# Kernel tuning notes

Measured on AMD Instinct MI355X. Metric: run time of the kernel, lower is better.

The kernel has to match this reference:

```python
import jax, jax.numpy as jnp
import numpy as np

N = 4096
IN = 64          # input_size
QD = 16          # query_vector_dim
CI = 2 * IN + 1  # 129, MLP_Param input dim


def _xavier(key, shape):
    fan_in, fan_out = shape[-2], shape[-1]
    bound = float(np.sqrt(6.0 / (fan_in + fan_out)))
    return jax.random.uniform(key, shape, jnp.float32, -bound, bound)


def setup_inputs() -> dict:
    key = jax.random.key(0)
    ks = jax.random.split(key, 10)
    return {
        "x": jax.random.normal(ks[0], (N, IN + 1), jnp.float32),
        "h": jax.random.normal(ks[1], (N, IN), jnp.float32),
        "query_vectors": jax.random.normal(ks[2], (N, QD), jnp.float32),
        "adj": jax.random.uniform(ks[3], (N, N), jnp.float32),
        "nodes_ind": jnp.arange(N, dtype=jnp.int64 if jax.config.jax_enable_x64 else jnp.int32),
        "W_r": _xavier(ks[4], (QD, CI, IN)),
        "b_r": _xavier(ks[5], (QD, IN)),
        "W_u": _xavier(ks[6], (QD, CI, IN)),
        "b_u": _xavier(ks[7], (QD, IN)),
        "W_c": _xavier(ks[8], (QD, CI, IN)),
        "b_c": _xavier(ks[9], (QD, IN)),
    }


def _mlp_param(xv, q, W, b):
    # per-node dynamic weights: [n, CI, IN]
    Wn = jnp.einsum('nd,dio->nio', q, W)
    return jnp.einsum('ni,nio->no', xv, Wn) + q @ b


def reference(x, h, query_vectors, adj, nodes_ind, W_r, b_r, W_u, b_u, W_c, b_c):
    combined = adj @ jnp.concatenate([x, h], axis=-1)          # [N, 129]
    cg = combined[nodes_ind]                                    # [M, 129]
    r = jax.nn.sigmoid(_mlp_param(cg, query_vectors, W_r, b_r))
    u = jax.nn.sigmoid(_mlp_param(cg, query_vectors, W_u, b_u))
    h2 = h.at[nodes_ind].set(r * h[nodes_ind])                  # h[nodes_ind] = r*h[nodes_ind]
    combined_new = jnp.concatenate([x, h2], axis=-1)[nodes_ind]  # no adj mixing second time
    cand = jnp.tanh(_mlp_param(combined_new, query_vectors, W_c, b_c))
    return (1.0 - u) * h2[nodes_ind] + u * cand
```

## Files before the change

kernel.cpp:

```cpp
#include <hip/hip_runtime.h>
#include <math.h>


#define NN   4096
#define XCC  65
#define HCC  64
#define QDIM 16
#define CI   129
#define CST  132
#define AKST 520
#define GSTRIDE 147456

typedef unsigned short u16;
typedef __attribute__((ext_vector_type(4))) unsigned short ushort4_t;
typedef __attribute__((ext_vector_type(8))) unsigned short ushort8_t;
typedef __attribute__((ext_vector_type(8))) short bf16x8;
typedef __attribute__((ext_vector_type(16))) float f32x16;

__device__ __forceinline__ void split2(float a, u16& hi, u16& lo) {
  unsigned u = __float_as_uint(a);
  hi = (u16)(u >> 16);
  float rec = __uint_as_float(u & 0xFFFF0000u);
  float lf = a - rec;
  unsigned v = __float_as_uint(lf);
  v += 0x7FFF + ((v >> 16) & 1);
  lo = (u16)(v >> 16);
}

__device__ __forceinline__ void gload_lds16(const void* gsrc, void* ldst) {
  __builtin_amdgcn_global_load_lds(
      (const __attribute__((address_space(1))) unsigned int*)gsrc,
      (__attribute__((address_space(3))) unsigned int*)ldst, 16, 0, 0);
}

__global__ __launch_bounds__(256) void k0_pack(const float* __restrict__ x,
                                               const float* __restrict__ h,
                                               u16* __restrict__ Bh,
                                               u16* __restrict__ Bl,
                                               const float* __restrict__ Wr,
                                               const float* __restrict__ Wu,
                                               const float* __restrict__ Wc,
                                               u16* __restrict__ Wh,
                                               u16* __restrict__ Wl) {
  __shared__ float sT[64][161];
  const int t = threadIdx.x;
  if (blockIdx.x < 64) {
    const int n0 = blockIdx.x * 64;
    for (int f = t; f < 64 * XCC; f += 256) {
      int n = f / XCC, c = f - n * XCC;
      sT[n][c] = x[(size_t)(n0 + n) * XCC + c];
    }
    for (int f = t; f < 64 * HCC; f += 256) {
      int n = f >> 6, c = f & 63;
      sT[n][XCC + c] = h[(size_t)(n0 + n) * HCC + c];
    }
    for (int f = t; f < 64 * 31; f += 256) {
      int n = f / 31, c = f - n * 31;
      sT[n][CI + c] = 0.f;
    }
    __syncthreads();
    for (int idx = t; idx < 5 * 4 * 64; idx += 256) {
      const int lane = idx & 63;
      const int ksl = (idx >> 6) & 3;
      const int ct = idx >> 8;
      const int nl = ksl * 16 + (lane >> 5) * 8;
      const int feat = ct * 32 + (lane & 31);
      ushort8_t vh, vl;
#pragma unroll
      for (int j = 0; j < 8; ++j) {
        u16 hi, lo; split2(sT[nl + j][feat], hi, lo);
        vh[j] = hi; vl[j] = lo;
      }
      const size_t off = (((size_t)ct * 256 + (blockIdx.x * 4) + ksl) * 64 + lane) * 8;
      *(ushort8_t*)(Bh + off) = vh;
      *(ushort8_t*)(Bl + off) = vl;
    }
  } else {
    int gid = (blockIdx.x - 64) * 256 + t;
    if (gid >= 3 * 16 * 2 * 9 * 64) return;
    int lane = gid & 63;
    int rest = gid >> 6;
    int kst = rest % 9; rest /= 9;
    int ct = rest & 1; rest >>= 1;
    int d = rest & 15; rest >>= 4;
    const float* W = (rest == 0) ? Wr : (rest == 1 ? Wu : Wc);
    const int o = ct * 32 + (lane & 31);
    const int i0 = kst * 16 + (lane >> 5) * 8;
    ushort8_t vh, vl;
#pragma unroll
    for (int j = 0; j < 8; ++j) {
      int i = i0 + j;
      float v = (i < CI) ? W[((size_t)d * CI + i) * 64 + o] : 0.f;
      u16 hi, lo; split2(v, hi, lo);
      vh[j] = hi; vl[j] = lo;
    }
    const size_t off = (size_t)gid * 8;
    *(ushort8_t*)(Wh + off) = vh;
    *(ushort8_t*)(Wl + off) = vl;
  }
}

template <int SPK>
__global__ __launch_bounds__(256, 4) void k1_mfma(const float* __restrict__ adj,
                                                  const u16* __restrict__ Bh,
                                                  const u16* __restrict__ Bl,
                                                  float* __restrict__ P1) {
  constexpr int KLEN = 4096 / SPK;
  constexpr int STEPS = KLEN / 16;
  __shared__ u16 sAh[2][2][64][8];
  __shared__ u16 sAl[2][2][64][8];
  __shared__ u16 sB[3][10][512];
  __shared__ u16 sScratch[512];
  const int t = threadIdx.x;
  const int lane = t & 63;
  const int w = t >> 6;
  const int rgrp = w & 1;
  const int cthalf = w >> 1;
  const int m0 = blockIdx.x * 64;
  const int sp = blockIdx.y;
  const int ct0 = cthalf ? 3 : 0;
  const int R = t >> 2;
  const int ksts = t & 3;
  const int srg = R >> 5, srl = R & 31;
  const int skh = ksts >> 1, sj0 = (ksts & 1) * 4;

  f32x16 a0, a1, a2;
#pragma unroll
  for (int r = 0; r < 16; ++r) { a0[r] = 0.f; a1[r] = 0.f; a2[r] = 0.f; }

  const float* aptr = adj + (size_t)(m0 + R) * NN + sp * KLEN + ksts * 4;
  float4 va, vb, vc;

#define LOADA(it, tgt) tgt = *(const float4*)(aptr + (it) * 16);

#define CONV4(src, abuf)                                                       \
  {                                                                            \
    u16 h0, h1, h2, h3, l0, l1, l2, l3;                                        \
    split2(src.x, h0, l0); split2(src.y, h1, l1);                              \
    split2(src.z, h2, l2); split2(src.w, h3, l3);                              \
    ushort4_t hv = {h0, h1, h2, h3};                                           \
    ushort4_t lv = {l0, l1, l2, l3};                                           \
    *(ushort4_t*)&sAh[abuf][srg][srl + 32 * skh][sj0] = hv;                    \
    *(ushort4_t*)&sAl[abuf][srg][srl + 32 * skh][sj0] = lv;                    \
  }

#define BDMA(it, bbuf)                                                         \
  {                                                                            \
    _Pragma("unroll")                                                          \
    for (int j = 0; j < 3; ++j) {                                              \
      const int c = w + 4 * j;                                                 \
      const int ct = (c < 10) ? (c >> 1) : 0;                                  \
      const int hl = (c < 10) ? (c & 1) : 0;                                   \
      const int ks = sp * STEPS + (it);                                        \
      const u16* src =                                                         \
          (hl ? Bl : Bh) + (((size_t)ct * 256 + ks) * 64 + lane) * 8;          \
      gload_lds16(src, (c < 10) ? &sB[bbuf][c][0] : &sScratch[0]);             \
    }                                                                          \
  }

#define BAR(N)                                                                 \
  asm volatile("s_waitcnt vmcnt(" #N ") lgkmcnt(0)" ::: "memory");             \
  __builtin_amdgcn_sched_barrier(0);                                           \
  __builtin_amdgcn_s_barrier();                                                \
  __builtin_amdgcn_sched_barrier(0);

#define COMPUTE(abuf, bbuf)                                                    \
  {                                                                            \
    bf16x8 ah = *(const bf16x8*)&sAh[abuf][rgrp][lane][0];                     \
    bf16x8 al = *(const bf16x8*)&sAl[abuf][rgrp][lane][0];                     \
    const int cb = ct0 * 2;                                                    \
    bf16x8 b0h = *(const bf16x8*)&sB[bbuf][cb + 0][lane * 8];                  \
    bf16x8 b0l = *(const bf16x8*)&sB[bbuf][cb + 1][lane * 8];                  \
    bf16x8 b1h = *(const bf16x8*)&sB[bbuf][cb + 2][lane * 8];                  \
    bf16x8 b1l = *(const bf16x8*)&sB[bbuf][cb + 3][lane * 8];                  \
    a0 = __builtin_amdgcn_mfma_f32_32x32x16_bf16(ah, b0h, a0, 0, 0, 0);        \
    a1 = __builtin_amdgcn_mfma_f32_32x32x16_bf16(ah, b1h, a1, 0, 0, 0);        \
    a0 = __builtin_amdgcn_mfma_f32_32x32x16_bf16(al, b0h, a0, 0, 0, 0);        \
    a1 = __builtin_amdgcn_mfma_f32_32x32x16_bf16(al, b1h, a1, 0, 0, 0);        \
    a0 = __builtin_amdgcn_mfma_f32_32x32x16_bf16(ah, b0l, a0, 0, 0, 0);        \
    a1 = __builtin_amdgcn_mfma_f32_32x32x16_bf16(ah, b1l, a1, 0, 0, 0);        \
    if (cthalf == 0) {                                                         \
      bf16x8 b2h = *(const bf16x8*)&sB[bbuf][cb + 4][lane * 8];                \
      bf16x8 b2l = *(const bf16x8*)&sB[bbuf][cb + 5][lane * 8];                \
      a2 = __builtin_amdgcn_mfma_f32_32x32x16_bf16(ah, b2h, a2, 0, 0, 0);      \
      a2 = __builtin_amdgcn_mfma_f32_32x32x16_bf16(al, b2h, a2, 0, 0, 0);      \
      a2 = __builtin_amdgcn_mfma_f32_32x32x16_bf16(ah, b2l, a2, 0, 0, 0);      \
    }                                                                          \
  }

  LOADA(0, va);
  BDMA(0, 0);
  LOADA(1, vb);
  BDMA(1, 1);
  LOADA(2, vc);
  CONV4(va, 0);
  BAR(5)
#pragma unroll
  for (int it = 0; it < STEPS; ++it) {
    const int abuf = it & 1;
    const int bbuf = it % 3;
    if (it < STEPS - 2) BDMA(it + 2, (it + 2) % 3);
    if (it <= STEPS - 4) {
      if ((it % 3) == 0) { LOADA(it + 3, va); }
      else if ((it % 3) == 1) { LOADA(it + 3, vb); }
      else { LOADA(it + 3, vc); }
    }
    COMPUTE(abuf, bbuf);
    if (it < STEPS - 1) {
      if (((it + 1) % 3) == 0) { CONV4(va, abuf ^ 1); }
      else if (((it + 1) % 3) == 1) { CONV4(vb, abuf ^ 1); }
      else { CONV4(vc, abuf ^ 1); }
    }
    if (it <= STEPS - 4) { BAR(5) }
    else if (it == STEPS - 3) { BAR(4) }
    else if (it == STEPS - 2) { BAR(0) }
  }
#undef LOADA
#undef CONV4
#undef BDMA
#undef BAR
#undef COMPUTE
  float* outp = P1 + (size_t)sp * NN * CST;
  const int colb = lane & 31;
  const int rbase = m0 + rgrp * 32 + 4 * (lane >> 5);
  {
    const int colg = ct0 * 32 + colb;
#pragma unroll
    for (int r = 0; r < 16; ++r)
      outp[(size_t)(rbase + (r & 3) + 8 * (r >> 2)) * CST + colg] = a0[r];
  }
  {
    const int colg = (ct0 + 1) * 32 + colb;
    if (colg < CST) {
#pragma unroll
      for (int r = 0; r < 16; ++r)
        outp[(size_t)(rbase + (r & 3) + 8 * (r >> 2)) * CST + colg] = a1[r];
    }
  }
  if (cthalf == 0) {
    const int colg = 64 + colb;
#pragma unroll
    for (int r = 0; r < 16; ++r)
      outp[(size_t)(rbase + (r & 3) + 8 * (r >> 2)) * CST + colg] = a2[r];
  }
}

template <int SPK>
__global__ void k1b_reduce(const float* __restrict__ P1, float* __restrict__ XV) {
  int f = blockIdx.x * 256 + threadIdx.x;
  if (f >= NN * 33) return;
  float sx = 0.f, sy = 0.f, sz = 0.f, sw = 0.f;
#pragma unroll
  for (int sp = 0; sp < SPK; ++sp) {
    float4 v = *(const float4*)(P1 + (size_t)sp * NN * CST + (size_t)f * 4);
    sx += v.x; sy += v.y; sz += v.z; sw += v.w;
  }
  float4 s = {sx, sy, sz, sw};
  *(float4*)(XV + (size_t)f * 4) = s;
}

__global__ __launch_bounds__(512) void k2_fused(const float* __restrict__ XV,
                                                const float* __restrict__ q,
                                                const u16* __restrict__ Wh,
                                                const u16* __restrict__ Wl,
                                                const float* __restrict__ br,
                                                const float* __restrict__ bu,
                                                const float* __restrict__ h,
                                                float* __restrict__ U,
                                                float* __restrict__ H2) {
  __shared__ float sXV[32][144];
  __shared__ u16 sAh[9 * AKST], sAl[9 * AKST];
  __shared__ float sQ[32][16];
  __shared__ float sXfer[8][16][64];
  const int t = threadIdx.x;
  const int n0 = blockIdx.x * 32;
  const int g = blockIdx.y >> 1, ct = blockIdx.y & 1;
  for (int f = t; f < 32 * 33; f += 512) {
    int n = f / 33, c4 = f - n * 33;
    *(float4*)&sXV[n][c4 * 4] = *(const float4*)(XV + (size_t)(n0 + n) * CST + c4 * 4);
  }
  for (int f = t; f < 32 * 3; f += 512) {
    float4 z = {0, 0, 0, 0};
    *(float4*)&sXV[f / 3][132 + (f % 3) * 4] = z;
  }
  if (t < 512) sQ[t >> 4][t & 15] = q[(size_t)(n0 + (t >> 4)) * QDIM + (t & 15)];
  __syncthreads();
  for (int s = t; s < 9 * 64; s += 512) {
    int kst = s >> 6, l = s & 63;
    int row = l & 31, k0 = kst * 16 + (l >> 5) * 8;
    ushort8_t vh, vl;
#pragma unroll
    for (int j = 0; j < 8; ++j) {
      u16 hi, lo; split2(sXV[row][k0 + j], hi, lo);
      vh[j] = hi; vl[j] = lo;
    }
    *(ushort8_t*)&sAh[kst * AKST + l * 8] = vh;
    *(ushort8_t*)&sAl[kst * AKST + l * 8] = vl;
  }
  __syncthreads();
  const int lane = t & 63, dh = t >> 6;
  const u16* WhG = Wh + (size_t)g * GSTRIDE;
  const u16* WlG = Wl + (size_t)g * GSTRIDE;
  f32x16 acc;
#pragma unroll
  for (int r = 0; r < 16; ++r) acc[r] = 0.f;
#pragma unroll
  for (int dd = 0; dd < 2; ++dd) {
    const int d = dh * 2 + dd;
    const size_t bb = (((size_t)d * 2 + ct) * 9 * 64 + lane) * 8;
    f32x16 t0, t1, t2;
#pragma unroll
    for (int r = 0; r < 16; ++r) { t0[r] = 0.f; t1[r] = 0.f; t2[r] = 0.f; }
#pragma unroll
    for (int kst = 0; kst < 9; ++kst) {
      bf16x8 ah = *(const bf16x8*)&sAh[kst * AKST + lane * 8];
      bf16x8 al = *(const bf16x8*)&sAl[kst * AKST + lane * 8];
      bf16x8 bh = *(const bf16x8*)(WhG + bb + kst * 512);
      bf16x8 bl = *(const bf16x8*)(WlG + bb + kst * 512);
      t0 = __builtin_amdgcn_mfma_f32_32x32x16_bf16(ah, bh, t0, 0, 0, 0);
      t1 = __builtin_amdgcn_mfma_f32_32x32x16_bf16(al, bh, t1, 0, 0, 0);
      t2 = __builtin_amdgcn_mfma_f32_32x32x16_bf16(ah, bl, t2, 0, 0, 0);
    }
#pragma unroll
    for (int r = 0; r < 16; ++r) {
      int node = (r & 3) + 8 * (r >> 2) + 4 * (lane >> 5);
      acc[r] += sQ[node][d] * (t0[r] + t1[r] + t2[r]);
    }
  }
#pragma unroll
  for (int r = 0; r < 16; ++r) sXfer[dh][r][lane] = acc[r];
  __syncthreads();
  if (dh == 0) {
    const int colb = ct * 32 + (lane & 31);
    const float* bias = (g == 0) ? br : bu;
    float bcol[16];
#pragma unroll
    for (int d = 0; d < 16; ++d) bcol[d] = bias[d * 64 + colb];
#pragma unroll
    for (int r = 0; r < 16; ++r) {
      int node = (r & 3) + 8 * (r >> 2) + 4 * (lane >> 5);
      float pre = 0.f;
#pragma unroll
      for (int wv = 0; wv < 8; ++wv) pre += sXfer[wv][r][lane];
#pragma unroll
      for (int d = 0; d < 16; ++d) pre += sQ[node][d] * bcol[d];
      float sg = 1.f / (1.f + expf(-pre));
      int gidx = (n0 + node) * 64 + colb;
      if (g == 0) H2[gidx] = sg * h[gidx];
      else U[gidx] = sg;
    }
  }
}

__global__ __launch_bounds__(512) void k3_fused(const float* __restrict__ x,
                                                const float* __restrict__ H2,
                                                const float* __restrict__ q,
                                                const u16* __restrict__ Wh,
                                                const u16* __restrict__ Wl,
                                                const float* __restrict__ bc,
                                                const float* __restrict__ U,
                                                float* __restrict__ out) {
  __shared__ float sXV[32][144];
  __shared__ u16 sAh[9 * AKST], sAl[9 * AKST];
  __shared__ float sQ[32][16];
  __shared__ float sXfer[8][16][64];
  const int t = threadIdx.x;
  const int n0 = blockIdx.x * 32;
  const int ct = blockIdx.y;
  for (int f = t; f < 32 * 144; f += 512) {
    int n = f / 144, i = f - n * 144;
    float v = 0.f;
    if (i < XCC) v = x[(size_t)(n0 + n) * XCC + i];
    else if (i < CI) v = H2[(size_t)(n0 + n) * HCC + (i - XCC)];
    sXV[n][i] = v;
  }
  if (t < 512) sQ[t >> 4][t & 15] = q[(size_t)(n0 + (t >> 4)) * QDIM + (t & 15)];
  __syncthreads();
  for (int s = t; s < 9 * 64; s += 512) {
    int kst = s >> 6, l = s & 63;
    int row = l & 31, k0 = kst * 16 + (l >> 5) * 8;
    ushort8_t vh, vl;
#pragma unroll
    for (int j = 0; j < 8; ++j) {
      u16 hi, lo; split2(sXV[row][k0 + j], hi, lo);
      vh[j] = hi; vl[j] = lo;
    }
    *(ushort8_t*)&sAh[kst * AKST + l * 8] = vh;
    *(ushort8_t*)&sAl[kst * AKST + l * 8] = vl;
  }
  __syncthreads();
  const int lane = t & 63, dh = t >> 6;
  const u16* WhG = Wh + (size_t)2 * GSTRIDE;
  const u16* WlG = Wl + (size_t)2 * GSTRIDE;
  f32x16 acc;
#pragma unroll
  for (int r = 0; r < 16; ++r) acc[r] = 0.f;
#pragma unroll
  for (int dd = 0; dd < 2; ++dd) {
    const int d = dh * 2 + dd;
    const size_t bb = (((size_t)d * 2 + ct) * 9 * 64 + lane) * 8;
    f32x16 t0, t1, t2;
#pragma unroll
    for (int r = 0; r < 16; ++r) { t0[r] = 0.f; t1[r] = 0.f; t2[r] = 0.f; }
#pragma unroll
    for (int kst = 0; kst < 9; ++kst) {
      bf16x8 ah = *(const bf16x8*)&sAh[kst * AKST + lane * 8];
      bf16x8 al = *(const bf16x8*)&sAl[kst * AKST + lane * 8];
      bf16x8 bh = *(const bf16x8*)(WhG + bb + kst * 512);
      bf16x8 bl = *(const bf16x8*)(WlG + bb + kst * 512);
      t0 = __builtin_amdgcn_mfma_f32_32x32x16_bf16(ah, bh, t0, 0, 0, 0);
      t1 = __builtin_amdgcn_mfma_f32_32x32x16_bf16(al, bh, t1, 0, 0, 0);
      t2 = __builtin_amdgcn_mfma_f32_32x32x16_bf16(ah, bl, t2, 0, 0, 0);
    }
#pragma unroll
    for (int r = 0; r < 16; ++r) {
      int node = (r & 3) + 8 * (r >> 2) + 4 * (lane >> 5);
      acc[r] += sQ[node][d] * (t0[r] + t1[r] + t2[r]);
    }
  }
#pragma unroll
  for (int r = 0; r < 16; ++r) sXfer[dh][r][lane] = acc[r];
  __syncthreads();
  if (dh == 0) {
    const int colb = ct * 32 + (lane & 31);
    float bcol[16];
#pragma unroll
    for (int d = 0; d < 16; ++d) bcol[d] = bc[d * 64 + colb];
#pragma unroll
    for (int r = 0; r < 16; ++r) {
      int node = (r & 3) + 8 * (r >> 2) + 4 * (lane >> 5);
      float pre = 0.f;
#pragma unroll
      for (int wv = 0; wv < 8; ++wv) pre += sXfer[wv][r][lane];
#pragma unroll
      for (int d = 0; d < 16; ++d) pre += sQ[node][d] * bcol[d];
      float cand = tanhf(pre);
      int gidx = (n0 + node) * 64 + colb;
      float u = U[gidx], h2 = H2[gidx];
      out[gidx] = (1.f - u) * h2 + u * cand;
    }
  }
}

extern "C" void kernel_launch(void* const* d_in, const int* in_sizes, int n_in,
                              void* d_out, int out_size, void* d_ws, size_t ws_size,
                              hipStream_t stream) {
  const float* x   = (const float*)d_in[0];
  const float* h   = (const float*)d_in[1];
  const float* q   = (const float*)d_in[2];
  const float* adj = (const float*)d_in[3];
  const float* Wr  = (const float*)d_in[5];
  const float* br  = (const float*)d_in[6];
  const float* Wu  = (const float*)d_in[7];
  const float* bu  = (const float*)d_in[8];
  const float* Wc  = (const float*)d_in[9];
  const float* bc  = (const float*)d_in[10];
  float* out = (float*)d_out;

  const size_t NEED16 = (size_t)16 * NN * CST * 4 + 2162688 + 10485760 + 1769472;
  const int spk = (ws_size >= NEED16) ? 16 : 8;

  char* ws = (char*)d_ws;
  const size_t OFF_P1 = 0;
  const size_t OFF_XV = OFF_P1 + (size_t)spk * NN * CST * 4;
  const size_t OFF_BP = OFF_XV + (size_t)NN * CST * 4;
  const size_t OFF_WH = OFF_BP + (size_t)2 * 5 * 256 * 64 * 8 * 2;
  const size_t OFF_WL = OFF_WH + (size_t)3 * GSTRIDE * 2;
  float* P1 = (float*)(ws + OFF_P1);
  float* XV = (float*)(ws + OFF_XV);
  u16*   Bh = (u16*)(ws + OFF_BP);
  u16*   Bl = (u16*)(ws + OFF_BP + (size_t)5 * 256 * 64 * 8 * 2);
  u16*   Wh = (u16*)(ws + OFF_WH);
  u16*   Wl = (u16*)(ws + OFF_WL);
  float* U  = (float*)(ws + OFF_P1 + 5242880);
  float* H2 = (float*)(ws + OFF_P1 + 6291456);

  hipLaunchKernelGGL(k0_pack, dim3(280), dim3(256), 0, stream,
                     x, h, Bh, Bl, Wr, Wu, Wc, Wh, Wl);
  if (spk == 16) {
    hipLaunchKernelGGL(k1_mfma<16>, dim3(64, 16), dim3(256), 0, stream, adj, Bh, Bl, P1);
    hipLaunchKernelGGL(k1b_reduce<16>, dim3(NN * 33 / 256), dim3(256), 0, stream, P1, XV);
  } else {
    hipLaunchKernelGGL(k1_mfma<8>, dim3(64, 8), dim3(256), 0, stream, adj, Bh, Bl, P1);
    hipLaunchKernelGGL(k1b_reduce<8>, dim3(NN * 33 / 256), dim3(256), 0, stream, P1, XV);
  }
  hipLaunchKernelGGL(k2_fused, dim3(128, 4), dim3(512), 0, stream, XV, q, Wh, Wl, br, bu, h, U, H2);
  hipLaunchKernelGGL(k3_fused, dim3(128, 2), dim3(512), 0, stream, x, H2, q, Wh, Wl, bc, U, out);
}
```

Before: 79.85 us.

## Fuse split-K reduce, gate, and candidate kernels into one per-node-tile kernel

Merges the split-K partial-sum reduction, the r/u gate MLP kernel and the candidate MLP kernel into a single kernel. Each block reads P1 directly, computes both r column halves itself so the full h2 row stays in shared memory, then runs the candidate MLP without a global round trip. This removes two launches and the XV/U/H2 global writes and reads. In exchange the r gate work is done twice, once per column-half block, the grid shrinks from 512 to 256 blocks, and extra barriers are added.

```diff
diff --git a/kernel.cpp b/kernel.cpp
--- a/kernel.cpp
+++ b/kernel.cpp
@@ -245,200 +245,145 @@
   }
 }
 
+
+#define PACKA()                                                                \
+  for (int s = t; s < 9 * 64; s += 512) {                                      \
+    int kst = s >> 6, l = s & 63;                                              \
+    int row = l & 31, k0i = kst * 16 + (l >> 5) * 8;                           \
+    ushort8_t vh, vl;                                                          \
+    _Pragma("unroll")                                                          \
+    for (int j = 0; j < 8; ++j) {                                              \
+      u16 hi, lo; split2(sXV[row][k0i + j], hi, lo);                           \
+      vh[j] = hi; vl[j] = lo;                                                  \
+    }                                                                          \
+    *(ushort8_t*)&sAh[kst * AKST + l * 8] = vh;                                \
+    *(ushort8_t*)&sAl[kst * AKST + l * 8] = vl;                                \
+  }
+
 template <int SPK>
-__global__ void k1b_reduce(const float* __restrict__ P1, float* __restrict__ XV) {
-  int f = blockIdx.x * 256 + threadIdx.x;
-  if (f >= NN * 33) return;
-  float sx = 0.f, sy = 0.f, sz = 0.f, sw = 0.f;
-#pragma unroll
-  for (int sp = 0; sp < SPK; ++sp) {
-    float4 v = *(const float4*)(P1 + (size_t)sp * NN * CST + (size_t)f * 4);
-    sx += v.x; sy += v.y; sz += v.z; sw += v.w;
-  }
-  float4 s = {sx, sy, sz, sw};
-  *(float4*)(XV + (size_t)f * 4) = s;
-}
-
-__global__ __launch_bounds__(512) void k2_fused(const float* __restrict__ XV,
-                                                const float* __restrict__ q,
-                                                const u16* __restrict__ Wh,
-                                                const u16* __restrict__ Wl,
-                                                const float* __restrict__ br,
-                                                const float* __restrict__ bu,
-                                                const float* __restrict__ h,
-                                                float* __restrict__ U,
-                                                float* __restrict__ H2) {
+__global__ __launch_bounds__(512) void k23_fused(
+    const float* __restrict__ P1, const float* __restrict__ x,
+    const float* __restrict__ h, const float* __restrict__ q,
+    const u16* __restrict__ Wh, const u16* __restrict__ Wl,
+    const float* __restrict__ br, const float* __restrict__ bu,
+    const float* __restrict__ bc, float* __restrict__ out) {
   __shared__ float sXV[32][144];
   __shared__ u16 sAh[9 * AKST], sAl[9 * AKST];
   __shared__ float sQ[32][16];
   __shared__ float sXfer[8][16][64];
   const int t = threadIdx.x;
   const int n0 = blockIdx.x * 32;
-  const int g = blockIdx.y >> 1, ct = blockIdx.y & 1;
+  const int cto = blockIdx.y;
   for (int f = t; f < 32 * 33; f += 512) {
     int n = f / 33, c4 = f - n * 33;
-    *(float4*)&sXV[n][c4 * 4] = *(const float4*)(XV + (size_t)(n0 + n) * CST + c4 * 4);
+    const float* p = P1 + (size_t)(n0 + n) * CST + c4 * 4;
+    float sx = 0.f, sy = 0.f, sz = 0.f, sw = 0.f;
+#pragma unroll
+    for (int sp = 0; sp < SPK; ++sp) {
+      float4 v = *(const float4*)(p + (size_t)sp * NN * CST);
+      sx += v.x; sy += v.y; sz += v.z; sw += v.w;
+    }
+    sXV[n][c4 * 4 + 0] = sx; sXV[n][c4 * 4 + 1] = sy;
+    sXV[n][c4 * 4 + 2] = sz; sXV[n][c4 * 4 + 3] = sw;
   }
   for (int f = t; f < 32 * 3; f += 512) {
     float4 z = {0, 0, 0, 0};
     *(float4*)&sXV[f / 3][132 + (f % 3) * 4] = z;
   }
-  if (t < 512) sQ[t >> 4][t & 15] = q[(size_t)(n0 + (t >> 4)) * QDIM + (t & 15)];
+  sQ[t >> 4][t & 15] = q[(size_t)(n0 + (t >> 4)) * QDIM + (t & 15)];
   __syncthreads();
-  for (int s = t; s < 9 * 64; s += 512) {
-    int kst = s >> 6, l = s & 63;
-    int row = l & 31, k0 = kst * 16 + (l >> 5) * 8;
-    ushort8_t vh, vl;
-#pragma unroll
-    for (int j = 0; j < 8; ++j) {
-      u16 hi, lo; split2(sXV[row][k0 + j], hi, lo);
-      vh[j] = hi; vl[j] = lo;
-    }
-    *(ushort8_t*)&sAh[kst * AKST + l * 8] = vh;
-    *(ushort8_t*)&sAl[kst * AKST + l * 8] = vl;
-  }
+  PACKA();
   __syncthreads();
+  for (int f = t; f < 32 * 65; f += 512) {
+    int n = f / 65, i = f - n * 65;
+    sXV[n][i] = x[(size_t)(n0 + n) * XCC + i];
+  }
   const int lane = t & 63, dh = t >> 6;
-  const u16* WhG = Wh + (size_t)g * GSTRIDE;
-  const u16* WlG = Wl + (size_t)g * GSTRIDE;
-  f32x16 acc;
-#pragma unroll
-  for (int r = 0; r < 16; ++r) acc[r] = 0.f;
-#pragma unroll
-  for (int dd = 0; dd < 2; ++dd) {
-    const int d = dh * 2 + dd;
-    const size_t bb = (((size_t)d * 2 + ct) * 9 * 64 + lane) * 8;
-    f32x16 t0, t1, t2;
-#pragma unroll
-    for (int r = 0; r < 16; ++r) { t0[r] = 0.f; t1[r] = 0.f; t2[r] = 0.f; }
-#pragma unroll
-    for (int kst = 0; kst < 9; ++kst) {
-      bf16x8 ah = *(const bf16x8*)&sAh[kst * AKST + lane * 8];
-      bf16x8 al = *(const bf16x8*)&sAl[kst * AKST + lane * 8];
-      bf16x8 bh = *(const bf16x8*)(WhG + bb + kst * 512);
-      bf16x8 bl = *(const bf16x8*)(WlG + bb + kst * 512);
-      t0 = __builtin_amdgcn_mfma_f32_32x32x16_bf16(ah, bh, t0, 0, 0, 0);
-      t1 = __builtin_amdgcn_mfma_f32_32x32x16_bf16(al, bh, t1, 0, 0, 0);
-      t2 = __builtin_amdgcn_mfma_f32_32x32x16_bf16(ah, bl, t2, 0, 0, 0);
-    }
-#pragma unroll
-    for (int r = 0; r < 16; ++r) {
-      int node = (r & 3) + 8 * (r >> 2) + 4 * (lane >> 5);
-      acc[r] += sQ[node][d] * (t0[r] + t1[r] + t2[r]);
-    }
-  }
-#pragma unroll
-  for (int r = 0; r < 16; ++r) sXfer[dh][r][lane] = acc[r];
+
+  auto mfma_target = [&](const u16* gh, const u16* gl, int ct_sel,
+                         float& o0, float& o1) {
+    f32x16 acc;
+#pragma unroll
+    for (int r = 0; r < 16; ++r) acc[r] = 0.f;
+#pragma unroll
+    for (int dd = 0; dd < 2; ++dd) {
+      const int d = dh * 2 + dd;
+      const size_t bb = (((size_t)d * 2 + ct_sel) * 9 * 64 + lane) * 8;
+      f32x16 t0, t1, t2;
+#pragma unroll
+      for (int r = 0; r < 16; ++r) { t0[r] = 0.f; t1[r] = 0.f; t2[r] = 0.f; }
+#pragma unroll
+      for (int kst = 0; kst < 9; ++kst) {
+        bf16x8 ah = *(const bf16x8*)&sAh[kst * AKST + lane * 8];
+        bf16x8 al = *(const bf16x8*)&sAl[kst * AKST + lane * 8];
+        bf16x8 bh = *(const bf16x8*)(gh + bb + kst * 512);
+        bf16x8 bl = *(const bf16x8*)(gl + bb + kst * 512);
+        t0 = __builtin_amdgcn_mfma_f32_32x32x16_bf16(ah, bh, t0, 0, 0, 0);
+        t1 = __builtin_amdgcn_mfma_f32_32x32x16_bf16(al, bh, t1, 0, 0, 0);
+        t2 = __builtin_amdgcn_mfma_f32_32x32x16_bf16(ah, bl, t2, 0, 0, 0);
+      }
+#pragma unroll
+      for (int r = 0; r < 16; ++r) {
+        int node = (r & 3) + 8 * (r >> 2) + 4 * (lane >> 5);
+        acc[r] += sQ[node][d] * (t0[r] + t1[r] + t2[r]);
+      }
+    }
+    __syncthreads();
+#pragma unroll
+    for (int r = 0; r < 16; ++r) sXfer[dh][r][lane] = acc[r];
+    __syncthreads();
+    const int rr0 = dh * 2, rr1 = dh * 2 + 1;
+    float s0 = 0.f, s1 = 0.f;
+#pragma unroll
+    for (int wv = 0; wv < 8; ++wv) {
+      s0 += sXfer[wv][rr0][lane];
+      s1 += sXfer[wv][rr1][lane];
+    }
+    o0 = s0; o1 = s1;
+  };
+
+  auto add_bias = [&](const float* bias, int node, int col, float pre) {
+#pragma unroll
+    for (int d = 0; d < 16; ++d) pre += sQ[node][d] * bias[(size_t)d * 64 + col];
+    return pre;
+  };
+
+  float r0p0, r0p1, r1p0, r1p1, up0, up1;
+  mfma_target(Wh, Wl, 0, r0p0, r0p1);
+  mfma_target(Wh, Wl, 1, r1p0, r1p1);
+  mfma_target(Wh + GSTRIDE, Wl + GSTRIDE, cto, up0, up1);
+
+  const int col0 = lane & 31, col1 = 32 + col0, colu = cto * 32 + col0;
+  float uval[2], h2own[2];
+#pragma unroll
+  for (int i = 0; i < 2; ++i) {
+    const int rr = dh * 2 + i;
+    const int node = (rr & 3) + 8 * (rr >> 2) + 4 * (lane >> 5);
+    float pr0 = add_bias(br, node, col0, i ? r0p1 : r0p0);
+    float pr1 = add_bias(br, node, col1, i ? r1p1 : r1p0);
+    float pu  = add_bias(bu, node, colu, i ? up1 : up0);
+    float rg0 = 1.f / (1.f + expf(-pr0));
+    float rg1 = 1.f / (1.f + expf(-pr1));
+    uval[i] = 1.f / (1.f + expf(-pu));
+    float h2a = rg0 * h[(size_t)(n0 + node) * HCC + col0];
+    float h2b = rg1 * h[(size_t)(n0 + node) * HCC + col1];
+    sXV[node][XCC + col0] = h2a;
+    sXV[node][XCC + col1] = h2b;
+    h2own[i] = cto ? h2b : h2a;
+  }
   __syncthreads();
-  if (dh == 0) {
-    const int colb = ct * 32 + (lane & 31);
-    const float* bias = (g == 0) ? br : bu;
-    float bcol[16];
-#pragma unroll
-    for (int d = 0; d < 16; ++d) bcol[d] = bias[d * 64 + colb];
-#pragma unroll
-    for (int r = 0; r < 16; ++r) {
-      int node = (r & 3) + 8 * (r >> 2) + 4 * (lane >> 5);
-      float pre = 0.f;
-#pragma unroll
-      for (int wv = 0; wv < 8; ++wv) pre += sXfer[wv][r][lane];
-#pragma unroll
-      for (int d = 0; d < 16; ++d) pre += sQ[node][d] * bcol[d];
-      float sg = 1.f / (1.f + expf(-pre));
-      int gidx = (n0 + node) * 64 + colb;
-      if (g == 0) H2[gidx] = sg * h[gidx];
-      else U[gidx] = sg;
-    }
-  }
-}
-
-__global__ __launch_bounds__(512) void k3_fused(const float* __restrict__ x,
-                                                const float* __restrict__ H2,
-                                                const float* __restrict__ q,
-                                                const u16* __restrict__ Wh,
-                                                const u16* __restrict__ Wl,
-                                                const float* __restrict__ bc,
-                                                const float* __restrict__ U,
-                                                float* __restrict__ out) {
-  __shared__ float sXV[32][144];
-  __shared__ u16 sAh[9 * AKST], sAl[9 * AKST];
-  __shared__ float sQ[32][16];
-  __shared__ float sXfer[8][16][64];
-  const int t = threadIdx.x;
-  const int n0 = blockIdx.x * 32;
-  const int ct = blockIdx.y;
-  for (int f = t; f < 32 * 144; f += 512) {
-    int n = f / 144, i = f - n * 144;
-    float v = 0.f;
-    if (i < XCC) v = x[(size_t)(n0 + n) * XCC + i];
-    else if (i < CI) v = H2[(size_t)(n0 + n) * HCC + (i - XCC)];
-    sXV[n][i] = v;
-  }
-  if (t < 512) sQ[t >> 4][t & 15] = q[(size_t)(n0 + (t >> 4)) * QDIM + (t & 15)];
+  PACKA();
   __syncthreads();
-  for (int s = t; s < 9 * 64; s += 512) {
-    int kst = s >> 6, l = s & 63;
-    int row = l & 31, k0 = kst * 16 + (l >> 5) * 8;
-    ushort8_t vh, vl;
-#pragma unroll
-    for (int j = 0; j < 8; ++j) {
-      u16 hi, lo; split2(sXV[row][k0 + j], hi, lo);
-      vh[j] = hi; vl[j] = lo;
-    }
-    *(ushort8_t*)&sAh[kst * AKST + l * 8] = vh;
-    *(ushort8_t*)&sAl[kst * AKST + l * 8] = vl;
-  }
-  __syncthreads();
-  const int lane = t & 63, dh = t >> 6;
-  const u16* WhG = Wh + (size_t)2 * GSTRIDE;
-  const u16* WlG = Wl + (size_t)2 * GSTRIDE;
-  f32x16 acc;
-#pragma unroll
-  for (int r = 0; r < 16; ++r) acc[r] = 0.f;
-#pragma unroll
-  for (int dd = 0; dd < 2; ++dd) {
-    const int d = dh * 2 + dd;
-    const size_t bb = (((size_t)d * 2 + ct) * 9 * 64 + lane) * 8;
-    f32x16 t0, t1, t2;
-#pragma unroll
-    for (int r = 0; r < 16; ++r) { t0[r] = 0.f; t1[r] = 0.f; t2[r] = 0.f; }
-#pragma unroll
-    for (int kst = 0; kst < 9; ++kst) {
-      bf16x8 ah = *(const bf16x8*)&sAh[kst * AKST + lane * 8];
-      bf16x8 al = *(const bf16x8*)&sAl[kst * AKST + lane * 8];
-      bf16x8 bh = *(const bf16x8*)(WhG + bb + kst * 512);
-      bf16x8 bl = *(const bf16x8*)(WlG + bb + kst * 512);
-      t0 = __builtin_amdgcn_mfma_f32_32x32x16_bf16(ah, bh, t0, 0, 0, 0);
-      t1 = __builtin_amdgcn_mfma_f32_32x32x16_bf16(al, bh, t1, 0, 0, 0);
-      t2 = __builtin_amdgcn_mfma_f32_32x32x16_bf16(ah, bl, t2, 0, 0, 0);
-    }
-#pragma unroll
-    for (int r = 0; r < 16; ++r) {
-      int node = (r & 3) + 8 * (r >> 2) + 4 * (lane >> 5);
-      acc[r] += sQ[node][d] * (t0[r] + t1[r] + t2[r]);
-    }
-  }
-#pragma unroll
-  for (int r = 0; r < 16; ++r) sXfer[dh][r][lane] = acc[r];
-  __syncthreads();
-  if (dh == 0) {
-    const int colb = ct * 32 + (lane & 31);
-    float bcol[16];
-#pragma unroll
-    for (int d = 0; d < 16; ++d) bcol[d] = bc[d * 64 + colb];
-#pragma unroll
-    for (int r = 0; r < 16; ++r) {
-      int node = (r & 3) + 8 * (r >> 2) + 4 * (lane >> 5);
-      float pre = 0.f;
-#pragma unroll
-      for (int wv = 0; wv < 8; ++wv) pre += sXfer[wv][r][lane];
-#pragma unroll
-      for (int d = 0; d < 16; ++d) pre += sQ[node][d] * bcol[d];
-      float cand = tanhf(pre);
-      int gidx = (n0 + node) * 64 + colb;
-      float u = U[gidx], h2 = H2[gidx];
-      out[gidx] = (1.f - u) * h2 + u * cand;
-    }
+  float cp0, cp1;
+  mfma_target(Wh + 2 * GSTRIDE, Wl + 2 * GSTRIDE, cto, cp0, cp1);
+#pragma unroll
+  for (int i = 0; i < 2; ++i) {
+    const int rr = dh * 2 + i;
+    const int node = (rr & 3) + 8 * (rr >> 2) + 4 * (lane >> 5);
+    float pc = add_bias(bc, node, colu, i ? cp1 : cp0);
+    float cand = tanhf(pc);
+    out[(size_t)(n0 + node) * HCC + colu] =
+        (1.f - uval[i]) * h2own[i] + uval[i] * cand;
   }
 }
 
@@ -467,23 +412,20 @@
   const size_t OFF_WH = OFF_BP + (size_t)2 * 5 * 256 * 64 * 8 * 2;
   const size_t OFF_WL = OFF_WH + (size_t)3 * GSTRIDE * 2;
   float* P1 = (float*)(ws + OFF_P1);
-  float* XV = (float*)(ws + OFF_XV);
   u16*   Bh = (u16*)(ws + OFF_BP);
   u16*   Bl = (u16*)(ws + OFF_BP + (size_t)5 * 256 * 64 * 8 * 2);
   u16*   Wh = (u16*)(ws + OFF_WH);
   u16*   Wl = (u16*)(ws + OFF_WL);
-  float* U  = (float*)(ws + OFF_P1 + 5242880);
-  float* H2 = (float*)(ws + OFF_P1 + 6291456);
 
   hipLaunchKernelGGL(k0_pack, dim3(280), dim3(256), 0, stream,
                      x, h, Bh, Bl, Wr, Wu, Wc, Wh, Wl);
   if (spk == 16) {
     hipLaunchKernelGGL(k1_mfma<16>, dim3(64, 16), dim3(256), 0, stream, adj, Bh, Bl, P1);
-    hipLaunchKernelGGL(k1b_reduce<16>, dim3(NN * 33 / 256), dim3(256), 0, stream, P1, XV);
+    hipLaunchKernelGGL(k23_fused<16>, dim3(128, 2), dim3(512), 0, stream,
+                       P1, x, h, q, Wh, Wl, br, bu, bc, out);
   } else {
     hipLaunchKernelGGL(k1_mfma<8>, dim3(64, 8), dim3(256), 0, stream, adj, Bh, Bl, P1);
-    hipLaunchKernelGGL(k1b_reduce<8>, dim3(NN * 33 / 256), dim3(256), 0, stream, P1, XV);
-  }
-  hipLaunchKernelGGL(k2_fused, dim3(128, 4), dim3(512), 0, stream, XV, q, Wh, Wl, br, bu, h, U, H2);
-  hipLaunchKernelGGL(k3_fused, dim3(128, 2), dim3(512), 0, stream, x, H2, q, Wh, Wl, bc, U, out);
-}
+    hipLaunchKernelGGL(k23_fused<8>, dim3(128, 2), dim3(512), 0, stream,
+                       P1, x, h, q, Wh, Wl, br, bu, bc, out);
+  }
+}
```

After: 67.88 us. 1.18x faster.
